# Performance work log

Hardware: AMD Instinct MI355X
Metric: run time of the kernel (lower is better)

Reference implementation:

```python
import jax, jax.numpy as jnp
import numpy as np

N_TOKENS = 100000
UNITS = 150  # CustomizeLSTMCell.TRANSITION_STATE_OUTPUTS_DIM


def setup_inputs() -> dict:
    key = jax.random.key(0)
    ks = jax.random.split(key, 9)
    f = lambda k, shape: jax.random.normal(k, shape, dtype=jnp.float32)
    return {
        "s_in": f(ks[0], (N_TOKENS, UNITS)),
        "s_out": f(ks[1], (N_TOKENS, UNITS)),
        "h_in": f(ks[2], (N_TOKENS, UNITS)),
        "h_out": f(ks[3], (N_TOKENS, UNITS)),
        "last_c": f(ks[4], (N_TOKENS, UNITS)),
        "w_in_input": f(ks[5], (UNITS, UNITS)) * 0.05,
        "w_out_input": f(ks[6], (UNITS, UNITS)) * 0.05,
        "u_in_input": f(ks[7], (UNITS, UNITS)) * 0.05,
        "u_out_input": f(ks[8], (UNITS, UNITS)) * 0.05,
    }


def reference(s_in, s_out, h_in, h_out, last_c,
              w_in_input, w_out_input, u_in_input, u_out_input):
    # Faithful to the source: all four gates use the *_input weights and no bias
    # (the original call() computes identical pre-activations for every gate).
    pre = (s_in @ w_in_input + s_out @ w_out_input
           + h_in @ u_in_input + h_out @ u_out_input)  # [N, H]
    gate = jax.nn.sigmoid(pre)
    # input_gate == output_gate == forget_gate == update_gate == gate
    cell_state = gate * last_c + gate * gate
    hidden_state = gate * jnp.tanh(cell_state)
    return hidden_state, cell_state
```

## Files before the change

kernel.cpp:

```cpp
#include <hip/hip_runtime.h>
#include <hip/hip_bf16.h>

typedef __attribute__((ext_vector_type(8))) short short8;
typedef __attribute__((ext_vector_type(4))) float f32x4;

#define NTOK   100000
#define H      150
#define NKS    20
#define BM     64
#define LBUF   18432
#define OUTOFF (NTOK * H)
#define AS1 __attribute__((address_space(1)))
#define AS3 __attribute__((address_space(3)))

__device__ __forceinline__ unsigned short f2bf(float f) {
    unsigned int u = __builtin_bit_cast(unsigned int, f);
    u = (u + 0x7FFFu + ((u >> 16) & 1u)) >> 16;
    return (unsigned short)u;
}

template<int N> __device__ __forceinline__ void vwait() {
    if constexpr (N == 6)      asm volatile("s_waitcnt vmcnt(6)" ::: "memory");
    else if constexpr (N == 4) asm volatile("s_waitcnt vmcnt(4)" ::: "memory");
    else if constexpr (N == 3) asm volatile("s_waitcnt vmcnt(3)" ::: "memory");
    else if constexpr (N == 2) asm volatile("s_waitcnt vmcnt(2)" ::: "memory");
    else                       asm volatile("s_waitcnt vmcnt(0)" ::: "memory");
}

__global__ void prep_w(const float* __restrict__ w_in, const float* __restrict__ w_out,
                       const float* __restrict__ u_in, const float* __restrict__ u_out,
                       unsigned short* __restrict__ wb) {
    int idx = blockIdx.x * 256 + threadIdx.x;
    if (idx >= NKS * 10 * 512) return;
    int j    = idx & 7;
    int lane = (idx >> 3) & 63;
    int n    = (idx >> 9) % 10;
    int ks   = idx / 5120;
    int seg  = ks / 5, s5 = ks % 5;
    int col  = n * 16 + (lane & 15);
    int p    = (lane >> 4) * 8 + j;
    int k2   = (s5 < 4) ? (s5 * 32 + p) : (120 + p);
    float v = 0.0f;
    if (col < H && k2 < H && !(s5 == 4 && p < 8)) {
        const float* W = (seg == 0) ? w_in : (seg == 1) ? w_out : (seg == 2) ? u_in : u_out;
        v = W[k2 * H + col];
    }
    wb[idx] = f2bf(v);
}

__global__ __launch_bounds__(512, 4) void lstm_fused(
        const float* __restrict__ s_in, const float* __restrict__ s_out,
        const float* __restrict__ h_in, const float* __restrict__ h_out,
        const float* __restrict__ last_c, const unsigned short* __restrict__ wb,
        float* __restrict__ out) {
    __shared__ __align__(16) char lds[4 * LBUF];

    const int t     = threadIdx.x;
    const int lane  = t & 63;
    const int wid   = t >> 6;
    const int waveM = wid >> 1;
    const int waveN = wid & 1;
    const int lrow  = lane & 15;
    const int lko   = lane >> 4;
    const int r0blk = blockIdx.x * BM;
    const bool tail = (r0blk + BM > NTOK);
    const bool cw3  = (wid < 2);

    const float* Xseg[4] = {s_in, s_out, h_in, h_out};

    f32x4 acc[5];
#pragma unroll
    for (int n = 0; n < 5; n++) acc[n] = (f32x4){0.f, 0.f, 0.f, 0.f};

    auto stage = [&](int ks2) {
        char* lb = &lds[(ks2 & 3) * LBUF];
        const int s5 = ks2 % 5;
        const int sofs = (s5 < 4) ? s5 * 128 : 480;
        {
            const char* xb = (const char*)Xseg[ks2 / 5];
            int rowg = r0blk + wid * 8 + (lane >> 3);
            if (rowg > NTOK - 1) rowg = NTOK - 1;
            const int q = (lane & 7) ^ ((lane >> 3) & 7);
            const long go = (long)rowg * 600 + sofs + q * 16;
            __builtin_amdgcn_global_load_lds(
                (const AS1 void*)(xb + go),
                (AS3 void*)(lb + wid * 1024 + lane * 16), 16, 0, 0);
        }
        {
            const char* bsrc = (const char*)wb + (long)ks2 * 10240;
            __builtin_amdgcn_global_load_lds(
                (const AS1 void*)(bsrc + wid * 1024 + lane * 16),
                (AS3 void*)(lb + 8192 + wid * 1024 + lane * 16), 16, 0, 0);
            if (cw3)
                __builtin_amdgcn_global_load_lds(
                    (const AS1 void*)(bsrc + (8 + wid) * 1024 + lane * 16),
                    (AS3 void*)(lb + 8192 + (8 + wid) * 1024 + lane * 16), 16, 0, 0);
        }
    };

    auto compute = [&](int ks2) {
        const char* lb = &lds[(ks2 & 3) * LBUF];
        const int row = waveM * 16 + lrow;
        const int r7 = lrow & 7;
        const char* xr = lb + row * 128;
        f32x4 v0 = *(const f32x4*)(xr + ((((lko << 1) | 0) ^ r7) << 4));
        f32x4 v1 = *(const f32x4*)(xr + ((((lko << 1) | 1) ^ r7) << 4));
        short8 af;
        af[0] = (short)f2bf(v0[0]); af[1] = (short)f2bf(v0[1]);
        af[2] = (short)f2bf(v0[2]); af[3] = (short)f2bf(v0[3]);
        af[4] = (short)f2bf(v1[0]); af[5] = (short)f2bf(v1[1]);
        af[6] = (short)f2bf(v1[2]); af[7] = (short)f2bf(v1[3]);
        const char* br = lb + 8192 + (waveN * 5) * 1024 + lane * 16;
#pragma unroll
        for (int n = 0; n < 5; n++) {
            short8 bf = *(const short8*)(br + n * 1024);
            acc[n] = __builtin_amdgcn_mfma_f32_16x16x32_bf16(af, bf, acc[n], 0, 0, 0);
        }
    };

    stage(0); stage(1); stage(2);

#pragma unroll
    for (int ks = 0; ks < NKS; ks++) {
        if (ks < NKS - 2)       { if (cw3) vwait<6>(); else vwait<4>(); }
        else if (ks == NKS - 2) { if (cw3) vwait<3>(); else vwait<2>(); }
        else                    vwait<0>();
        __builtin_amdgcn_s_barrier();
        asm volatile("" ::: "memory");

        if (tail && (ks % 5) == 4) {
            if (wid == 0 && lane < 33) {
                const int slot = 31 + lane;
                const int r7s = slot & 7;
                *(float2*)&lds[(ks & 3) * LBUF + slot * 128 + ((7 ^ r7s) << 4) + 8]
                    = make_float2(0.f, 0.f);
            }
            asm volatile("s_waitcnt lgkmcnt(0)" ::: "memory");
            __builtin_amdgcn_s_barrier();
            asm volatile("" ::: "memory");
        }

        if (ks < NKS - 3) stage(ks + 3);
        compute(ks);
    }

#pragma unroll
    for (int r = 0; r < 4; r++) {
        const int row = r0blk + waveM * 16 + lko * 4 + r;
        if (row >= NTOK) continue;
        const long rb = (long)row * H;
#pragma unroll
        for (int n = 0; n < 5; n++) {
            const int col = waveN * 80 + n * 16 + lrow;
            if (col >= H) continue;
            float pre = acc[n][r];
            float e   = __expf(-pre);
            float g   = __builtin_amdgcn_rcpf(1.f + e);
            float lc  = last_c[rb + col];
            float cell = g * lc + g * g;
            float e2  = __expf(-2.f * cell);
            float th  = (1.f - e2) * __builtin_amdgcn_rcpf(1.f + e2);
            out[rb + col]          = g * th;
            out[OUTOFF + rb + col] = cell;
        }
    }
}

extern "C" void kernel_launch(void* const* d_in, const int* in_sizes, int n_in,
                              void* d_out, int out_size, void* d_ws, size_t ws_size,
                              hipStream_t stream) {
    const float* s_in   = (const float*)d_in[0];
    const float* s_out  = (const float*)d_in[1];
    const float* h_in   = (const float*)d_in[2];
    const float* h_out  = (const float*)d_in[3];
    const float* last_c = (const float*)d_in[4];
    const float* w_in   = (const float*)d_in[5];
    const float* w_out  = (const float*)d_in[6];
    const float* u_in   = (const float*)d_in[7];
    const float* u_out  = (const float*)d_in[8];

    unsigned short* wb = (unsigned short*)d_ws;
    float* out = (float*)d_out;

    prep_w<<<(NKS * 10 * 512 + 255) / 256, 256, 0, stream>>>(w_in, w_out, u_in, u_out, wb);

    const int nblocks = (NTOK + BM - 1) / BM;
    lstm_fused<<<nblocks, 512, 0, stream>>>(s_in, s_out, h_in, h_out, last_c, wb, out);
}
```

Baseline: 122.2 us.

## Prefetch last_c into registers during the K loop and drop the tail-zeroing barrier

Issues the last_c loads for the epilogue during the third-to-last K step, so their latency overlaps the final MFMA steps instead of stalling the epilogue. The vmcnt waits are adjusted to account for the 20 extra outstanding loads. The last K slice now reads from an offset that stays inside the row, with the weight rows for the overlap zeroed, which removes the tail-block LDS zeroing and its extra barrier. It also raises wave priority around the MFMA sequence. The cost is 20 more live registers per thread, which may hurt occupancy at launch bounds of 512 threads and 4 blocks.

```diff
diff --git a/kernel.cpp b/kernel.cpp
--- a/kernel.cpp
+++ b/kernel.cpp
@@ -20,11 +20,12 @@
 }
 
 template<int N> __device__ __forceinline__ void vwait() {
-    if constexpr (N == 6)      asm volatile("s_waitcnt vmcnt(6)" ::: "memory");
-    else if constexpr (N == 4) asm volatile("s_waitcnt vmcnt(4)" ::: "memory");
-    else if constexpr (N == 3) asm volatile("s_waitcnt vmcnt(3)" ::: "memory");
-    else if constexpr (N == 2) asm volatile("s_waitcnt vmcnt(2)" ::: "memory");
-    else                       asm volatile("s_waitcnt vmcnt(0)" ::: "memory");
+    if constexpr (N == 6)       asm volatile("s_waitcnt vmcnt(6)" ::: "memory");
+    else if constexpr (N == 4)  asm volatile("s_waitcnt vmcnt(4)" ::: "memory");
+    else if constexpr (N == 23) asm volatile("s_waitcnt vmcnt(23)" ::: "memory");
+    else if constexpr (N == 22) asm volatile("s_waitcnt vmcnt(22)" ::: "memory");
+    else if constexpr (N == 20) asm volatile("s_waitcnt vmcnt(20)" ::: "memory");
+    else                        asm volatile("s_waitcnt vmcnt(0)" ::: "memory");
 }
 
 __global__ void prep_w(const float* __restrict__ w_in, const float* __restrict__ w_out,
@@ -39,9 +40,9 @@
     int seg  = ks / 5, s5 = ks % 5;
     int col  = n * 16 + (lane & 15);
     int p    = (lane >> 4) * 8 + j;
-    int k2   = (s5 < 4) ? (s5 * 32 + p) : (120 + p);
+    int k2   = (s5 < 4) ? (s5 * 32 + p) : (118 + p);
     float v = 0.0f;
-    if (col < H && k2 < H && !(s5 == 4 && p < 8)) {
+    if (col < H && !(s5 == 4 && p < 10)) {
         const float* W = (seg == 0) ? w_in : (seg == 1) ? w_out : (seg == 2) ? u_in : u_out;
         v = W[k2 * H + col];
     }
@@ -63,7 +64,6 @@
     const int lrow  = lane & 15;
     const int lko   = lane >> 4;
     const int r0blk = blockIdx.x * BM;
-    const bool tail = (r0blk + BM > NTOK);
     const bool cw3  = (wid < 2);
 
     const float* Xseg[4] = {s_in, s_out, h_in, h_out};
@@ -72,10 +72,12 @@
 #pragma unroll
     for (int n = 0; n < 5; n++) acc[n] = (f32x4){0.f, 0.f, 0.f, 0.f};
 
+    float lcv[4][5];
+
     auto stage = [&](int ks2) {
         char* lb = &lds[(ks2 & 3) * LBUF];
         const int s5 = ks2 % 5;
-        const int sofs = (s5 < 4) ? s5 * 128 : 480;
+        const int sofs = (s5 < 4) ? s5 * 128 : 472;
         {
             const char* xb = (const char*)Xseg[ks2 / 5];
             int rowg = r0blk + wid * 8 + (lane >> 3);
@@ -111,38 +113,45 @@
         af[4] = (short)f2bf(v1[0]); af[5] = (short)f2bf(v1[1]);
         af[6] = (short)f2bf(v1[2]); af[7] = (short)f2bf(v1[3]);
         const char* br = lb + 8192 + (waveN * 5) * 1024 + lane * 16;
+        __builtin_amdgcn_s_setprio(1);
 #pragma unroll
         for (int n = 0; n < 5; n++) {
             short8 bf = *(const short8*)(br + n * 1024);
             acc[n] = __builtin_amdgcn_mfma_f32_16x16x32_bf16(af, bf, acc[n], 0, 0, 0);
         }
+        __builtin_amdgcn_s_setprio(0);
     };
 
     stage(0); stage(1); stage(2);
 
 #pragma unroll
     for (int ks = 0; ks < NKS; ks++) {
-        if (ks < NKS - 2)       { if (cw3) vwait<6>(); else vwait<4>(); }
-        else if (ks == NKS - 2) { if (cw3) vwait<3>(); else vwait<2>(); }
-        else                    vwait<0>();
+        if (ks < NKS - 2)       { if (cw3) vwait<6>();  else vwait<4>();  }
+        else if (ks == NKS - 2) { if (cw3) vwait<23>(); else vwait<22>(); }
+        else                    vwait<20>();
         __builtin_amdgcn_s_barrier();
         asm volatile("" ::: "memory");
 
-        if (tail && (ks % 5) == 4) {
-            if (wid == 0 && lane < 33) {
-                const int slot = 31 + lane;
-                const int r7s = slot & 7;
-                *(float2*)&lds[(ks & 3) * LBUF + slot * 128 + ((7 ^ r7s) << 4) + 8]
-                    = make_float2(0.f, 0.f);
+        if (ks < NKS - 3) stage(ks + 3);
+
+        if (ks == NKS - 3) {
+#pragma unroll
+            for (int r = 0; r < 4; r++) {
+                int row = r0blk + waveM * 16 + lko * 4 + r;
+                if (row > NTOK - 1) row = NTOK - 1;
+#pragma unroll
+                for (int n = 0; n < 5; n++) {
+                    int col = waveN * 80 + n * 16 + lrow;
+                    if (col >= H) col = 0;
+                    lcv[r][n] = last_c[(long)row * H + col];
+                }
             }
-            asm volatile("s_waitcnt lgkmcnt(0)" ::: "memory");
-            __builtin_amdgcn_s_barrier();
-            asm volatile("" ::: "memory");
         }
 
-        if (ks < NKS - 3) stage(ks + 3);
         compute(ks);
     }
+
+    vwait<0>();
 
 #pragma unroll
     for (int r = 0; r < 4; r++) {
@@ -156,8 +165,7 @@
             float pre = acc[n][r];
             float e   = __expf(-pre);
             float g   = __builtin_amdgcn_rcpf(1.f + e);
-            float lc  = last_c[rb + col];
-            float cell = g * lc + g * g;
+            float cell = g * lcv[r][n] + g * g;
             float e2  = __expf(-2.f * cell);
             float th  = (1.f - e2) * __builtin_amdgcn_rcpf(1.f + e2);
             out[rb + col]          = g * th;
```

After: 113.7 us, median of 2. -6.9%, faster.
